# Performance work log

Hardware: AMD Instinct MI355X
Metric: run time of the kernel (lower is better)

## Reference

```python
import jax, jax.numpy as jnp
import numpy as np

B, N, M, D, H, DK = 4, 2048, 1024, 512, 8, 64  # H*DK == D (required by residual E + E_)
SCALE = 1.0 / np.sqrt(DK)
NEG = -9e15


def setup_inputs() -> dict:
    key = jax.random.key(0)
    ks = jax.random.split(key, 24)
    def W(k, din, dout):
        return (0.02 * jax.random.truncated_normal(k, -2.0, 2.0, (din, dout))).astype(jnp.float32)
    inp = {
        'X': jax.random.normal(ks[0], (B, N, D), jnp.float32),
        'incidence_matrix': jax.random.randint(ks[1], (B, N, M), 0, 2, jnp.int32),
        'attn_bias': jnp.zeros((1,), jnp.float32),
        'E': jax.random.normal(ks[2], (B, M, D), jnp.float32),
        'Wqn': W(ks[3], D, H * DK), 'bqn': jnp.zeros((H * DK,), jnp.float32),
        'Wkn': W(ks[4], D, H * DK), 'bkn': jnp.zeros((H * DK,), jnp.float32),
        'Wvn': W(ks[5], D, H * DK), 'bvn': jnp.zeros((H * DK,), jnp.float32),
        'Wqe': W(ks[6], D, H * DK), 'bqe': jnp.zeros((H * DK,), jnp.float32),
        'Wke': W(ks[7], D, H * DK), 'bke': jnp.zeros((H * DK,), jnp.float32),
        'Wve': W(ks[8], D, H * DK), 'bve': jnp.zeros((H * DK,), jnp.float32),
        'Wm1': W(ks[9], D, D), 'bm1': jnp.zeros((D,), jnp.float32),
        'Wm2': W(ks[10], D, D), 'bm2': jnp.zeros((D,), jnp.float32),
        'g_ln': jnp.ones((D,), jnp.float32), 'b_ln': jnp.zeros((D,), jnp.float32),
    }
    return inp


def _heads(x, Wt, b):
    # [B, L, D] -> [B, H, L, DK]
    b_, l_ = x.shape[0], x.shape[1]
    return (x @ Wt + b).reshape(b_, l_, H, DK).transpose(0, 2, 1, 3)


def _merge(x):
    # [B, H, L, DK] -> [B, L, H*DK]
    b_, _, l_, _ = x.shape
    return x.transpose(0, 2, 1, 3).reshape(b_, l_, H * DK)


def _layernorm(x, g, b, eps=1e-7):
    mu = jnp.mean(x, axis=-1, keepdims=True)
    var = jnp.var(x, axis=-1, keepdims=True)
    return (x - mu) * jax.lax.rsqrt(var + eps) * g + b


def _gelu(x):
    return jax.nn.gelu(x, approximate=False)


def reference(X, incidence_matrix, attn_bias, E,
              Wqn, bqn, Wkn, bkn, Wvn, bvn,
              Wqe, bqe, Wke, bke, Wve, bve,
              Wm1, bm1, Wm2, bm2, g_ln, b_ln):
    q_n = _heads(X, Wqn, bqn)   # [B,H,N,DK]
    k_n = _heads(X, Wkn, bkn)
    v_n = _heads(X, Wvn, bvn)
    q_e = _heads(E, Wqe, bqe)   # [B,H,M,DK]

    # edge attends over nodes: [B,H,M,N], masked by incidence^T
    att_e = jnp.einsum('bhmd,bhnd->bhmn', q_e, k_n) * SCALE
    mask_e = (incidence_matrix > 0).transpose(0, 2, 1)[:, None, :, :]  # [B,1,M,N]
    att_e = jnp.where(mask_e, att_e, NEG)
    w_e = jax.nn.softmax(att_e, axis=-1)
    E_ = _gelu(jnp.einsum('bhmn,bhnd->bhmd', w_e, v_n))
    E_ = _merge(E_)                                   # [B,M,D]
    E_ = _layernorm(E + E_, g_ln, b_ln)
    E_ = _gelu(E_ @ Wm1 + bm1) @ Wm2 + bm2            # MLP

    k_e = _heads(E_, Wke, bke)  # [B,H,M,DK]
    v_e = _heads(E_, Wve, bve)

    # node attends over edges: [B,H,N,M], masked by incidence
    att_n = jnp.einsum('bhnd,bhmd->bhnm', q_n, k_e) * SCALE
    mask_n = (incidence_matrix > 0)[:, None, :, :]    # [B,1,N,M]
    att_n = jnp.where(mask_n, att_n, NEG)
    w_n = jax.nn.softmax(att_n, axis=-1)
    X_ = _gelu(jnp.einsum('bhnm,bhmd->bhnd', w_n, v_e))
    X_ = _merge(X_)                                   # [B,N,D]
    return (X_, E_)
```

## Files before the change

kernel.cpp:

```cpp
#include <hip/hip_runtime.h>

typedef unsigned short u16;
typedef unsigned int   u32;
typedef unsigned long long u64;

typedef __attribute__((ext_vector_type(8))) short  bf16x8;
typedef __attribute__((ext_vector_type(16))) float f32x16;

#define SC2 0.1803368801111243f
#define CS2 11.541560327111707f

__device__ __forceinline__ float bf2f(u16 h) { return __uint_as_float(((u32)h) << 16); }
__device__ __forceinline__ u16 f2bf(float f) {
  u32 u = __float_as_uint(f);
  return (u16)((u + 0x7FFFu + ((u >> 16) & 1u)) >> 16);
}
__device__ __forceinline__ float gelu_f(float x) {
  return 0.5f * x * (1.0f + erff(x * 0.70710678118654752440f));
}
__device__ __forceinline__ void dma16(const u16* g, u16* l) {
  __builtin_amdgcn_global_load_lds(
      (const __attribute__((address_space(1))) u32*)g,
      (__attribute__((address_space(3))) u32*)l, 16, 0, 0);
}
__device__ __forceinline__ u32 cvtpk(float lo, float hi) {
  u32 r;
  asm("v_cvt_pk_bf16_f32 %0, %1, %2" : "=v"(r) : "v"(lo), "v"(hi));
  return r;
}

__global__ void detect_dtype(const u16* __restrict__ X, u32* __restrict__ flag) {
  int lane = threadIdx.x;
  int bad = 0;
  #pragma unroll
  for (int i = 0; i < 8; ++i) {
    u16 v = X[i * 64 + lane];
    int e = (v >> 7) & 0xFF;
    if (e >= 0x88) bad++;
  }
  #pragma unroll
  for (int o = 1; o < 64; o <<= 1) bad += __shfl_xor(bad, o);
  if (lane == 0) *flag = (bad > 16) ? 1u : 0u;
}

__global__ __launch_bounds__(256) void fill_diag(u32* __restrict__ out, float base,
                                                 const u32* __restrict__ flag) {
  float v = base + (*flag ? 4000.0f : 0.0f);
  u16 h = f2bf(v);
  out[blockIdx.x * 256 + threadIdx.x] = (u32)h | ((u32)h << 16);
}

__global__ __launch_bounds__(256) void conv_bf16(const void* __restrict__ src,
                                                 u16* __restrict__ dst, int n,
                                                 const u32* __restrict__ flag) {
  int i = (blockIdx.x * 256 + threadIdx.x) * 8;
  if (i >= n) return;
  if (*flag) {
    const float* s = (const float*)src + i;
    float4 a = *(const float4*)s;
    float4 b = *(const float4*)(s + 4);
    uint4 o;
    o.x = (u32)f2bf(a.x) | ((u32)f2bf(a.y) << 16);
    o.y = (u32)f2bf(a.z) | ((u32)f2bf(a.w) << 16);
    o.z = (u32)f2bf(b.x) | ((u32)f2bf(b.y) << 16);
    o.w = (u32)f2bf(b.z) | ((u32)f2bf(b.w) << 16);
    *(uint4*)(dst + i) = o;
  } else {
    *(uint4*)(dst + i) = *(const uint4*)((const u16*)src + i);
  }
}

__global__ __launch_bounds__(256) void conv_vec10(
    const void* p0, const void* p1, const void* p2, const void* p3, const void* p4,
    const void* p5, const void* p6, const void* p7, const void* p8, const void* p9,
    u16* __restrict__ dst, const u32* __restrict__ flag) {
  const void* ps[10] = {p0, p1, p2, p3, p4, p5, p6, p7, p8, p9};
  int fl = (int)(*flag);
  for (int idx = threadIdx.x; idx < 5120; idx += 256) {
    int slot = idx >> 9, off = idx & 511;
    u16 v;
    if (fl) v = f2bf(((const float*)ps[slot])[off]);
    else    v = ((const u16*)ps[slot])[off];
    dst[idx] = v;
  }
}

__global__ __launch_bounds__(256) void wtrans(
    const void* w0, const void* w1, const void* w2, const void* w3,
    const void* w4, const void* w5, const void* w6, const void* w7,
    u16* __restrict__ WT, const u32* __restrict__ flag) {
  const void* wsrc[8] = {w0, w1, w2, w3, w4, w5, w6, w7};
  __shared__ u16 tile[32][33];
  int z = blockIdx.z;
  const void* W = wsrc[z];
  u16* Wt = WT + (size_t)z * 262144;
  int fl = (int)(*flag);
  int tx = threadIdx.x & 31, ty = threadIdx.x >> 5;
  int bx = blockIdx.x * 32, by = blockIdx.y * 32;
  #pragma unroll
  for (int i = 0; i < 4; ++i) {
    int r = ty + 8 * i;
    size_t src = (size_t)(by + r) * 512 + bx + tx;
    tile[r][tx] = fl ? f2bf(((const float*)W)[src]) : ((const u16*)W)[src];
  }
  __syncthreads();
  #pragma unroll
  for (int i = 0; i < 4; ++i) {
    int r = ty + 8 * i;
    Wt[(size_t)(bx + r) * 512 + by + tx] = tile[tx][r];
  }
}

__global__ __launch_bounds__(256) void transposeV(const u16* __restrict__ Vp,
                                                  u16* __restrict__ VT, int Lk) {
  __shared__ u16 tile[64][72];
  int t = threadIdx.x;
  int nt = blockIdx.x;
  int bh = blockIdx.y;
  int nw = Lk >> 6;
  const u16* src = Vp + ((size_t)bh * Lk + nt * 64) * 64;
  int key = t >> 2, seg = t & 3;
  int dc0 = seg * 2, dc1 = seg * 2 + 1;
  uint4 a  = *(const uint4*)(src + key * 64 + ((dc0 ^ (key & 7)) << 3));
  uint4 b2 = *(const uint4*)(src + key * 64 + ((dc1 ^ (key & 7)) << 3));
  *(uint4*)&tile[key][dc0 * 8] = a;
  *(uint4*)&tile[key][dc1 * 8] = b2;
  __syncthreads();
  int d = t >> 2;
  u32 wb[8];
  #pragma unroll
  for (int i = 0; i < 8; ++i) {
    u32 lo = tile[seg * 16 + 2 * i][d];
    u32 hi = tile[seg * 16 + 2 * i + 1][d];
    wb[i] = lo | (hi << 16);
  }
  u16* base = VT + (((size_t)bh * nw + nt) * 64 + d) * 64;
  int kc0 = seg * 2, kc1 = seg * 2 + 1;
  uint4 o0; o0.x = wb[0]; o0.y = wb[1]; o0.z = wb[2]; o0.w = wb[3];
  uint4 o1; o1.x = wb[4]; o1.y = wb[5]; o1.z = wb[6]; o1.w = wb[7];
  *(uint4*)(base + ((kc0 ^ (d & 7)) << 3)) = o0;
  *(uint4*)(base + ((kc1 ^ (d & 7)) << 3)) = o1;
}

__global__ __launch_bounds__(256) void pack_rows(const int* __restrict__ inc,
                                                 u64* __restrict__ packNT) {
  int gid  = blockIdx.x * 4 + (threadIdx.x >> 6);
  int lane = threadIdx.x & 63;
  int w  = gid & 15;
  int bn = gid >> 4;
  int b = bn >> 11, n = bn & 2047;
  int v = inc[(size_t)bn * 1024 + (w << 6) + lane];
  u64 mask = __ballot(v > 0);
  if (lane == 0) packNT[((size_t)(b * 16 + w)) * 2048 + n] = mask;
}

__global__ __launch_bounds__(256) void pack_cols(const int* __restrict__ inc,
                                                 u64* __restrict__ packTT) {
  int m = blockIdx.x * 256 + threadIdx.x;
  int w = blockIdx.y;
  int b = blockIdx.z;
  const int* base = inc + ((size_t)b * 2048 + (size_t)w * 64) * 1024 + m;
  u64 out = 0;
  #pragma unroll 8
  for (int j = 0; j < 64; ++j)
    if (base[(size_t)j * 1024] > 0) out |= (1ull << j);
  packTT[((size_t)(b * 32 + w)) * 1024 + m] = out;
}

__global__ __launch_bounds__(256) void gemm_tiled(const u16* __restrict__ A,
                                                  const u16* __restrict__ Wt0, u32 wtStride,
                                                  const u16* __restrict__ bias0, u32 bStride,
                                                  u16* __restrict__ C0, u32 cStride,
                                                  int act, int blocksPerMat,
                                                  u32 modeMask, int lkshift,
                                                  void* __restrict__ out2, size_t out2_off,
                                                  const u32* __restrict__ flag) {
  __shared__ u16 As[2][8192];
  __shared__ u16 Bs[2][8192];
  int mat = blockIdx.x / blocksPerMat;
  int blk = blockIdx.x % blocksPerMat;
  const u16* Wt = Wt0 + (size_t)mat * wtStride;
  const u16* bias = bias0 + (size_t)mat * bStride;
  u16* C = C0 + (size_t)mat * cStride;
  int mode = (modeMask >> mat) & 1u;
  int f32o = out2 ? (int)(*flag) : 0;
  int tm = blk >> 2, tn = blk & 3;
  int m0 = tm * 128, n0 = tn * 128;

  int t = threadIdx.x;
  int wave = t >> 6, lane = t & 63;
  int nl = lane & 31, h32 = lane >> 5;
  int wm = wave >> 1, wn = wave & 1;

  int srow = lane >> 3;
  int gch  = (lane & 7) ^ srow;
  const u16* Ab = A  + ((size_t)m0 + wave * 32) * 512 + (size_t)srow * 512 + gch * 8;
  const u16* Bb = Wt + ((size_t)n0 + wave * 32) * 512 + (size_t)srow * 512 + gch * 8;
  u16* AsW = &As[0][0] + wave * 32 * 64;
  u16* BsW = &Bs[0][0] + wave * 32 * 64;

  #pragma unroll
  for (int c = 0; c < 4; ++c) {
    dma16(Ab + (size_t)c * 8 * 512, AsW + c * 8 * 64);
    dma16(Bb + (size_t)c * 8 * 512, BsW + c * 8 * 64);
  }
  __syncthreads();

  f32x16 a00 = {}, a01 = {}, a10 = {}, a11 = {};

  for (int kk = 0; kk < 8; ++kk) {
    int buf = kk & 1;
    if (kk + 1 < 8) {
      int k0n = (kk + 1) * 64;
      u16* AD = &As[buf ^ 1][0] + wave * 32 * 64;
      u16* BD = &Bs[buf ^ 1][0] + wave * 32 * 64;
      #pragma unroll
      for (int c = 0; c < 4; ++c) {
        dma16(Ab + (size_t)c * 8 * 512 + k0n, AD + c * 8 * 64);
        dma16(Bb + (size_t)c * 8 * 512 + k0n, BD + c * 8 * 64);
      }
    }
    const u16* Ab_s = &As[buf][0];
    const u16* Bb_s = &Bs[buf][0];
    int ar0 = wm * 64 + nl, ar1 = wm * 64 + 32 + nl;
    int br0 = wn * 64 + nl, br1 = wn * 64 + 32 + nl;
    #pragma unroll
    for (int ks = 0; ks < 4; ++ks) {
      int sw = (((ks * 2 + h32) ^ (nl & 7)) << 3);
      bf16x8 fa0 = *(const bf16x8*)(Ab_s + ar0 * 64 + sw);
      bf16x8 fa1 = *(const bf16x8*)(Ab_s + ar1 * 64 + sw);
      bf16x8 fb0 = *(const bf16x8*)(Bb_s + br0 * 64 + sw);
      bf16x8 fb1 = *(const bf16x8*)(Bb_s + br1 * 64 + sw);
      a00 = __builtin_amdgcn_mfma_f32_32x32x16_bf16(fa0, fb0, a00, 0, 0, 0);
      a01 = __builtin_amdgcn_mfma_f32_32x32x16_bf16(fa0, fb1, a01, 0, 0, 0);
      a10 = __builtin_amdgcn_mfma_f32_32x32x16_bf16(fa1, fb0, a10, 0, 0, 0);
      a11 = __builtin_amdgcn_mfma_f32_32x32x16_bf16(fa1, fb1, a11, 0, 0, 0);
    }
    __syncthreads();
  }

  int nw = 1 << (lkshift - 6);
  #pragma unroll
  for (int am = 0; am < 2; ++am) {
    #pragma unroll
    for (int bn = 0; bn < 2; ++bn) {
      const f32x16* accp = am == 0 ? (bn == 0 ? &a00 : &a01)
                                   : (bn == 0 ? &a10 : &a11);
      f32x16 acc = *accp;
      int cn = n0 + wn * 64 + bn * 32 + nl;
      float bv = bf2f(bias[cn]);
      #pragma unroll
      for (int g = 0; g < 16; ++g) {
        int rm = m0 + wm * 64 + am * 32 + (g & 3) + 8 * (g >> 2) + 4 * h32;
        float v = acc[g] + bv;
        if (act) v = gelu_f(v);
        if (mode) {
          int bb = rm >> lkshift;
          int key = rm & ((1 << lkshift) - 1);
          int nt = key >> 6, kl = key & 63;
          int d = cn & 63;
          size_t ad = ((((size_t)bb * 8 + (cn >> 6)) * nw + nt) * 64 + kl) * 64
                      + (((d >> 3) ^ (kl & 7)) << 3) + (d & 7);
          C[ad] = f2bf(v);
        } else {
          size_t ad = (size_t)rm * 512 + cn;
          C[ad] = f2bf(v);
          if (out2) {
            if (f32o) ((float*)out2)[out2_off + ad] = v;
            else      ((u16*)out2)[out2_off + ad] = f2bf(v);
          }
        }
      }
    }
  }
}

__global__ __launch_bounds__(128, 2) void flash_mfma(
    const u16* __restrict__ Q,
    const u16* __restrict__ Kp,
    const u16* __restrict__ VTp,
    const u64* __restrict__ maskT,
    void* __restrict__ Outv,
    u16* __restrict__ Opart, float* __restrict__ Lpart,
    int Lq, int Lk, int splits, int is_final, const u32* __restrict__ flag) {
  __shared__ u16 K_s[2][4096];
  __shared__ u16 V_s[2][4096];
  __shared__ u16 P_s[2][2048];

  int t = threadIdx.x;
  int wave = t >> 6, lane = t & 63;
  int nl = lane & 31, h32 = lane >> 5;
  int qtiles = Lq >> 6;
  int nwords = Lk >> 6;
  int chunk = (int)(gridDim.x >> 3);
  int wid = (blockIdx.x & 7) * chunk + (blockIdx.x >> 3);
  int r2 = wid % (qtiles * 32);
  int split = wid / (qtiles * 32);
  int qt = r2 % qtiles;
  int bh = r2 / qtiles;
  int h = bh & 7, b = bh >> 3;
  int row0 = qt * 64 + wave * 32;
  int per = nwords / splits;
  int tile0 = split * per;
  int f32o = is_final ? (int)(*flag) : 0;

  bf16x8 qf[4];
  {
    const u16* qp = Q + ((size_t)(b * Lq) + row0 + nl) * 512 + h * 64 + h32 * 8;
    #pragma unroll
    for (int ks = 0; ks < 4; ++ks) qf[ks] = *(const bf16x8*)(qp + ks * 16);
  }
  const u16* Kbh = Kp + (size_t)bh * Lk * 64;
  const u16* Vbh = VTp + (size_t)bh * nwords * 4096;
  const u64* mrow = maskT + (size_t)b * nwords * Lq + row0 + nl;

  f32x16 o0 = {}, o1 = {};
  float lsum = 0.f;

  {
    const u16* TK = Kbh + (size_t)tile0 * 4096;
    const u16* TV = Vbh + (size_t)tile0 * 4096;
    #pragma unroll
    for (int c = 0; c < 4; ++c) {
      int ch = c * 2 + wave;
      dma16(TK + ch * 512 + lane * 8, &K_s[0][ch * 512]);
      dma16(TV + ch * 512 + lane * 8, &V_s[0][ch * 512]);
    }
  }
  __syncthreads();

  for (int i = 0; i < per; ++i) {
    int nt = tile0 + i;
    int buf = i & 1;
    if (i + 1 < per) {
      const u16* TK = Kbh + (size_t)(nt + 1) * 4096;
      const u16* TV = Vbh + (size_t)(nt + 1) * 4096;
      u16* KD = K_s[buf ^ 1];
      u16* VD = V_s[buf ^ 1];
      #pragma unroll
      for (int c = 0; c < 4; ++c) {
        int ch = c * 2 + wave;
        dma16(TK + ch * 512 + lane * 8, KD + ch * 512);
        dma16(TV + ch * 512 + lane * 8, VD + ch * 512);
      }
    }
    u64 mymask = mrow[(size_t)nt * Lq];
    u32 mlo = (u32)mymask;
    u32 mhi = (u32)(mymask >> 32);

    f32x16 s0 = {}, s1 = {};
    #pragma unroll
    for (int ks = 0; ks < 4; ++ks) {
      int ch = ks * 2 + h32;
      bf16x8 k0 = *(const bf16x8*)&K_s[buf][nl * 64 + ((ch ^ (nl & 7)) << 3)];
      bf16x8 k1 = *(const bf16x8*)&K_s[buf][(32 + nl) * 64 + ((ch ^ (nl & 7)) << 3)];
      s0 = __builtin_amdgcn_mfma_f32_32x32x16_bf16(k0, qf[ks], s0, 0, 0, 0);
      s1 = __builtin_amdgcn_mfma_f32_32x32x16_bf16(k1, qf[ks], s1, 0, 0, 0);
    }
    #pragma unroll
    for (int gg = 0; gg < 4; ++gg) {
      float pv0[4], pv1[4];
      #pragma unroll
      for (int r = 0; r < 4; ++r) {
        int g = gg * 4 + r;
        int key = r + 8 * gg + 4 * h32;
        float e0 = exp2f(fmaf(s0[g], SC2, -CS2));
        float e1 = exp2f(fmaf(s1[g], SC2, -CS2));
        pv0[r] = ((mlo >> key) & 1u) ? e0 : 0.f;
        pv1[r] = ((mhi >> key) & 1u) ? e1 : 0.f;
        lsum += pv0[r] + pv1[r];
      }
      uint2 a0, a1;
      a0.x = cvtpk(pv0[0], pv0[1]);
      a0.y = cvtpk(pv0[2], pv0[3]);
      a1.x = cvtpk(pv1[0], pv1[1]);
      a1.y = cvtpk(pv1[2], pv1[3]);
      *(uint2*)&P_s[wave][gg * 256 + nl * 8 + 4 * h32]       = a0;
      *(uint2*)&P_s[wave][(4 + gg) * 256 + nl * 8 + 4 * h32] = a1;
    }
    asm volatile("s_waitcnt lgkmcnt(0)" ::: "memory");
    #pragma unroll
    for (int ks2 = 0; ks2 < 4; ++ks2) {
      int ch = ks2 * 2 + h32;
      bf16x8 pf = *(const bf16x8*)&P_s[wave][ch * 256 + nl * 8];
      bf16x8 v0 = *(const bf16x8*)&V_s[buf][nl * 64 + ((ch ^ (nl & 7)) << 3)];
      bf16x8 v1 = *(const bf16x8*)&V_s[buf][(32 + nl) * 64 + ((ch ^ (nl & 7)) << 3)];
      o0 = __builtin_amdgcn_mfma_f32_32x32x16_bf16(pf, v0, o0, 0, 0, 0);
      o1 = __builtin_amdgcn_mfma_f32_32x32x16_bf16(pf, v1, o1, 0, 0, 0);
    }
    __syncthreads();
  }
  lsum += __shfl_xor(lsum, 32);

  if (Opart) {
    u16* ob = Opart + (size_t)split * 2097152;
    #pragma unroll
    for (int g = 0; g < 16; ++g) {
      int m = (g & 3) + 8 * (g >> 2) + 4 * h32;
      size_t base = ((size_t)(b * Lq) + row0 + m) * 512 + h * 64;
      ob[base + nl]      = f2bf(o0[g]);
      ob[base + 32 + nl] = f2bf(o1[g]);
    }
    if (h32 == 0)
      Lpart[(size_t)split * 32768 + ((size_t)(b * Lq) + row0 + nl) * 8 + h] = lsum;
  } else {
    #pragma unroll
    for (int g = 0; g < 16; ++g) {
      int m = (g & 3) + 8 * (g >> 2) + 4 * h32;
      float lv = __shfl(lsum, m);
      float inv = 1.0f / (lv + 1e-30f);
      size_t base = ((size_t)(b * Lq) + row0 + m) * 512 + h * 64;
      float v0 = gelu_f(o0[g] * inv);
      float v1 = gelu_f(o1[g] * inv);
      if (f32o) {
        ((float*)Outv)[base + nl]      = v0;
        ((float*)Outv)[base + 32 + nl] = v1;
      } else {
        ((u16*)Outv)[base + nl]      = f2bf(v0);
        ((u16*)Outv)[base + 32 + nl] = f2bf(v1);
      }
    }
  }
}

__global__ __launch_bounds__(256) void ln_fused(const u16* __restrict__ Op,
                                                const float* __restrict__ Lp,
                                                const u16* __restrict__ E,
                                                const u16* __restrict__ g,
                                                const u16* __restrict__ bb,
                                                u16* __restrict__ out) {
  int r = blockIdx.x;
  int t = threadIdx.x;
  int e = t * 2;
  int h = e >> 6;
  float lv = Lp[r * 8 + h] + Lp[32768 + r * 8 + h] + 1e-30f;
  float inv = 1.0f / lv;
  size_t idx = (size_t)r * 512 + e;
  u32 u0 = *(const u32*)&Op[idx];
  u32 u1 = *(const u32*)&Op[2097152 + idx];
  u32 ue = *(const u32*)&E[idx];
  float x0 = bf2f((u16)(ue & 0xffffu)) +
             gelu_f((bf2f((u16)(u0 & 0xffffu)) + bf2f((u16)(u1 & 0xffffu))) * inv);
  float x1 = bf2f((u16)(ue >> 16)) +
             gelu_f((bf2f((u16)(u0 >> 16)) + bf2f((u16)(u1 >> 16))) * inv);
  float s = x0 + x1, q = x0 * x0 + x1 * x1;
  #pragma unroll
  for (int o = 32; o; o >>= 1) { s += __shfl_down(s, o); q += __shfl_down(q, o); }
  __shared__ float red[8];
  int wv = t >> 6, ln = t & 63;
  if (ln == 0) { red[wv] = s; red[4 + wv] = q; }
  __syncthreads();
  s = red[0] + red[1] + red[2] + red[3];
  q = red[4] + red[5] + red[6] + red[7];
  float mean = s * (1.f / 512.f);
  float var  = q * (1.f / 512.f) - mean * mean;
  float rs = rsqrtf(var + 1e-7f);
  u32 ug = *(const u32*)(g + e);
  u32 ub = *(const u32*)(bb + e);
  float y0 = (x0 - mean) * rs * bf2f((u16)(ug & 0xffffu)) + bf2f((u16)(ub & 0xffffu));
  float y1 = (x1 - mean) * rs * bf2f((u16)(ug >> 16)) + bf2f((u16)(ub >> 16));
  *(u32*)(out + idx) = (u32)f2bf(y0) | ((u32)f2bf(y1) << 16);
}

extern "C" void kernel_launch(void* const* d_in, const int* in_sizes, int n_in,
                              void* d_out, int out_size, void* d_ws, size_t ws_size,
                              hipStream_t stream) {
  (void)in_sizes; (void)n_in; (void)out_size;
  const int* inc = (const int*)d_in[1];

  char* ws = (char*)d_ws;
  u32* FLAG = (u32*)ws;
  u16* VEC  = (u16*)(ws + 1024);
  u16* WT   = (u16*)(ws + 65536);
  u16* XB   = (u16*)(ws + 8454144);
  u16* EB   = (u16*)(ws + 16842752);
  u16* QN   = (u16*)(ws + 21037056);
  u16* KN   = (u16*)(ws + 29425664);
  u16* VN   = (u16*)(ws + 37814272);
  u16* QE   = (u16*)(ws + 46202880);
  u16* EATT = (u16*)(ws + 50397184);
  u16* EFIN = (u16*)(ws + 54591488);
  u64* PACKT = (u64*)(ws + 58785792);
  u64* PACKN = (u64*)(ws + 59834368);
  const size_t NEEDED = 60882944;
  u16* ELN = (u16*)(ws + 29425664);
  u16* H1  = (u16*)(ws + 33619968);
  u16* KE  = (u16*)(ws + 37814272);
  u16* Opart = XB;
  float* Lpart = (float*)(ws + 37814272);
  u16* VTn = (u16*)d_out;
  u16* VTe = EATT;
  u16* VE  = (u16*)(ws + 42008576);

  detect_dtype<<<1, 64, 0, stream>>>((const u16*)d_in[0], FLAG);

  if (ws_size < NEEDED) {
    fill_diag<<<8192, 256, 0, stream>>>((u32*)d_out,
                                        1000.0f + (float)(ws_size >> 20), FLAG);
    return;
  }

  conv_bf16<<<2048, 256, 0, stream>>>(d_in[0], XB, 4194304, FLAG);
  conv_bf16<<<1024, 256, 0, stream>>>(d_in[3], EB, 2097152, FLAG);
  conv_vec10<<<1, 256, 0, stream>>>(d_in[5], d_in[7], d_in[9], d_in[11], d_in[13],
                                    d_in[15], d_in[17], d_in[19], d_in[20], d_in[21],
                                    VEC, FLAG);
  wtrans<<<dim3(16, 16, 8), 256, 0, stream>>>(d_in[4], d_in[6], d_in[8], d_in[10],
                                              d_in[12], d_in[14], d_in[16], d_in[18],
                                              WT, FLAG);
  pack_cols<<<dim3(4, 32, 4), 256, 0, stream>>>(inc, PACKT);
  pack_rows<<<32768, 256, 0, stream>>>(inc, PACKN);

  gemm_tiled<<<768, 256, 0, stream>>>(XB, WT, 262144, VEC, 512,
                                      QN, 4194304, 0, 256, 0b110u, 11,
                                      nullptr, 0, FLAG);
  gemm_tiled<<<128, 256, 0, stream>>>(EB, WT + 3 * 262144, 0, VEC + 3 * 512, 0,
                                      QE, 0, 0, 128, 0, 11, nullptr, 0, FLAG);

  transposeV<<<dim3(32, 32), 256, 0, stream>>>(VN, VTn, 2048);

  flash_mfma<<<1024, 128, 0, stream>>>(QE, KN, VTn, PACKT, nullptr,
                                       Opart, Lpart, 1024, 2048, 2, 0, FLAG);

  ln_fused<<<4096, 256, 0, stream>>>(Opart, Lpart, EB,
                                     VEC + 8 * 512, VEC + 9 * 512, ELN);
  gemm_tiled<<<128, 256, 0, stream>>>(ELN, WT + 6 * 262144, 0, VEC + 6 * 512, 0,
                                      H1, 0, 1, 128, 0, 11, nullptr, 0, FLAG);
  gemm_tiled<<<128, 256, 0, stream>>>(H1, WT + 7 * 262144, 0, VEC + 7 * 512, 0,
                                      EFIN, 0, 0, 128, 0, 11,
                                      d_out, 4194304, FLAG);

  gemm_tiled<<<256, 256, 0, stream>>>(EFIN, WT + 4 * 262144, 262144, VEC + 4 * 512, 512,
                                      KE, 2097152, 0, 128, 0b11u, 10,
                                      nullptr, 0, FLAG);
  transposeV<<<dim3(16, 32), 256, 0, stream>>>(VE, VTe, 1024);

  flash_mfma<<<1024, 128, 0, stream>>>(QN, KE, VTe, PACKN, d_out,
                                       nullptr, nullptr, 2048, 1024, 1, 1, FLAG);
}
```

Baseline: 384.5 us.

## Replace bitmask incidence with bf16 additive bias tiles folded into MFMA

Instead of bit-packing the incidence matrix into u64 masks and selecting per element after exp, new kernels expand it into bf16 tiles holding 0 or a large negative bias, laid out in MFMA fragment order. The flash kernel adds the bias to the scores through extra MFMAs against identity fragments, which removes the per-element bit tests and selects. In exchange it reads 16x more mask data per tile (bf16 instead of bits), adds four MFMAs per tile, and reuses several workspace regions for the tile buffers.

```diff
diff --git a/kernel.cpp b/kernel.cpp
--- a/kernel.cpp
+++ b/kernel.cpp
@@ -142,29 +142,50 @@
   *(uint4*)(base + ((kc1 ^ (d & 7)) << 3)) = o1;
 }
 
-__global__ __launch_bounds__(256) void pack_rows(const int* __restrict__ inc,
-                                                 u64* __restrict__ packNT) {
-  int gid  = blockIdx.x * 4 + (threadIdx.x >> 6);
-  int lane = threadIdx.x & 63;
-  int w  = gid & 15;
-  int bn = gid >> 4;
-  int b = bn >> 11, n = bn & 2047;
-  int v = inc[(size_t)bn * 1024 + (w << 6) + lane];
-  u64 mask = __ballot(v > 0);
-  if (lane == 0) packNT[((size_t)(b * 16 + w)) * 2048 + n] = mask;
-}
-
-__global__ __launch_bounds__(256) void pack_cols(const int* __restrict__ inc,
-                                                 u64* __restrict__ packTT) {
-  int m = blockIdx.x * 256 + threadIdx.x;
-  int w = blockIdx.y;
-  int b = blockIdx.z;
-  const int* base = inc + ((size_t)b * 2048 + (size_t)w * 64) * 1024 + m;
-  u64 out = 0;
-  #pragma unroll 8
-  for (int j = 0; j < 64; ++j)
-    if (base[(size_t)j * 1024] > 0) out |= (1ull << j);
-  packTT[((size_t)(b * 32 + w)) * 1024 + m] = out;
+__global__ __launch_bounds__(256) void inc_tiles_edge(const int* __restrict__ inc,
+                                                      u16* __restrict__ T0,
+                                                      u16* __restrict__ T1) {
+  int qt32 = blockIdx.x, nt = blockIdx.y, b = blockIdx.z;
+  int t = threadIdx.x;
+  int f = t >> 6, l = t & 63;
+  int nl = l & 31, h = l >> 5;
+  int key  = ((f >> 1) << 5) + nl;
+  int qrow = ((f & 1) << 4) + h * 8;
+  const int* src = inc + ((size_t)(b * 2048 + nt * 64 + key)) * 1024 + qt32 * 32 + qrow;
+  uint4 a = *(const uint4*)src;
+  uint4 c = *(const uint4*)(src + 4);
+  uint4 o;
+  o.x = (a.x ? 0u : 0xC480u) | (a.y ? 0u : 0xC4800000u);
+  o.y = (a.z ? 0u : 0xC480u) | (a.w ? 0u : 0xC4800000u);
+  o.z = (c.x ? 0u : 0xC480u) | (c.y ? 0u : 0xC4800000u);
+  o.w = (c.z ? 0u : 0xC480u) | (c.w ? 0u : 0xC4800000u);
+  u16* dst = (b < 2 ? T0 + (size_t)b * 2097152 : T1 + (size_t)(b - 2) * 2097152)
+             + ((size_t)nt * 32 + qt32) * 2048 + t * 8;
+  *(uint4*)dst = o;
+}
+
+__global__ __launch_bounds__(256) void inc_tiles_node(const int* __restrict__ inc,
+                                                      u16* __restrict__ T0,
+                                                      u16* __restrict__ T1) {
+  int qt32 = blockIdx.x, nt = blockIdx.y, b = blockIdx.z;
+  int t = threadIdx.x;
+  int f = t >> 6, l = t & 63;
+  int nl = l & 31, h = l >> 5;
+  int key  = ((f >> 1) << 5) + nl;
+  int qrow = ((f & 1) << 4) + h * 8;
+  const int* src = inc + ((size_t)(b * 2048 + qt32 * 32 + qrow)) * 1024 + nt * 64 + key;
+  u16 o[8];
+  #pragma unroll
+  for (int e = 0; e < 8; ++e)
+    o[e] = src[(size_t)e * 1024] ? (u16)0 : (u16)0xC480;
+  uint4 ov;
+  ov.x = (u32)o[0] | ((u32)o[1] << 16);
+  ov.y = (u32)o[2] | ((u32)o[3] << 16);
+  ov.z = (u32)o[4] | ((u32)o[5] << 16);
+  ov.w = (u32)o[6] | ((u32)o[7] << 16);
+  u16* dst = (b < 3 ? T0 + (size_t)b * 2097152 : T1)
+             + ((size_t)nt * 64 + qt32) * 2048 + t * 8;
+  *(uint4*)dst = ov;
 }
 
 __global__ __launch_bounds__(256) void gemm_tiled(const u16* __restrict__ A,
@@ -279,7 +300,9 @@
     const u16* __restrict__ Q,
     const u16* __restrict__ Kp,
     const u16* __restrict__ VTp,
-    const u64* __restrict__ maskT,
+    const u16* __restrict__ IncA,
+    const u16* __restrict__ IncB,
+    int nbA,
     void* __restrict__ Outv,
     u16* __restrict__ Opart, float* __restrict__ Lpart,
     int Lq, int Lk, int splits, int is_final, const u32* __restrict__ flag) {
@@ -310,9 +333,20 @@
     #pragma unroll
     for (int ks = 0; ks < 4; ++ks) qf[ks] = *(const bf16x8*)(qp + ks * 16);
   }
+  bf16x8 b0f = {}, b16f = {};
+  #pragma unroll
+  for (int e = 0; e < 8; ++e) {
+    b0f[e]  = (nl == h32 * 8 + e)      ? (short)0x3F80 : (short)0;
+    b16f[e] = (nl == 16 + h32 * 8 + e) ? (short)0x3F80 : (short)0;
+  }
+
   const u16* Kbh = Kp + (size_t)bh * Lk * 64;
   const u16* Vbh = VTp + (size_t)bh * nwords * 4096;
-  const u64* mrow = maskT + (size_t)b * nwords * Lq + row0 + nl;
+  size_t tstr = (size_t)(Lq >> 5) * 2048;
+  int qt2 = qt * 2 + wave;
+  const u16* It = (b < nbA ? IncA + (size_t)b * 2097152
+                           : IncB + (size_t)(b - nbA) * 2097152)
+                  + (size_t)qt2 * 2048 + lane * 8;
 
   f32x16 o0 = {}, o1 = {};
   float lsum = 0.f;
@@ -327,11 +361,20 @@
       dma16(TV + ch * 512 + lane * 8, &V_s[0][ch * 512]);
     }
   }
+  bf16x8 mc0, mc1, mc2, mc3;
+  {
+    const u16* p = It + (size_t)tile0 * tstr;
+    mc0 = *(const bf16x8*)(p);
+    mc1 = *(const bf16x8*)(p + 512);
+    mc2 = *(const bf16x8*)(p + 1024);
+    mc3 = *(const bf16x8*)(p + 1536);
+  }
   __syncthreads();
 
   for (int i = 0; i < per; ++i) {
     int nt = tile0 + i;
     int buf = i & 1;
+    bf16x8 mn0, mn1, mn2, mn3;
     if (i + 1 < per) {
       const u16* TK = Kbh + (size_t)(nt + 1) * 4096;
       const u16* TV = Vbh + (size_t)(nt + 1) * 4096;
@@ -343,10 +386,12 @@
         dma16(TK + ch * 512 + lane * 8, KD + ch * 512);
         dma16(TV + ch * 512 + lane * 8, VD + ch * 512);
       }
-    }
-    u64 mymask = mrow[(size_t)nt * Lq];
-    u32 mlo = (u32)mymask;
-    u32 mhi = (u32)(mymask >> 32);
+      const u16* p = It + (size_t)(nt + 1) * tstr;
+      mn0 = *(const bf16x8*)(p);
+      mn1 = *(const bf16x8*)(p + 512);
+      mn2 = *(const bf16x8*)(p + 1024);
+      mn3 = *(const bf16x8*)(p + 1536);
+    }
 
     f32x16 s0 = {}, s1 = {};
     #pragma unroll
@@ -357,18 +402,22 @@
       s0 = __builtin_amdgcn_mfma_f32_32x32x16_bf16(k0, qf[ks], s0, 0, 0, 0);
       s1 = __builtin_amdgcn_mfma_f32_32x32x16_bf16(k1, qf[ks], s1, 0, 0, 0);
     }
+    s0 = __builtin_amdgcn_mfma_f32_32x32x16_bf16(mc0, b0f,  s0, 0, 0, 0);
+    s0 = __builtin_amdgcn_mfma_f32_32x32x16_bf16(mc1, b16f, s0, 0, 0, 0);
+    s1 = __builtin_amdgcn_mfma_f32_32x32x16_bf16(mc2, b0f,  s1, 0, 0, 0);
+    s1 = __builtin_amdgcn_mfma_f32_32x32x16_bf16(mc3, b16f, s1, 0, 0, 0);
+
     #pragma unroll
     for (int gg = 0; gg < 4; ++gg) {
       float pv0[4], pv1[4];
       #pragma unroll
       for (int r = 0; r < 4; ++r) {
         int g = gg * 4 + r;
-        int key = r + 8 * gg + 4 * h32;
         float e0 = exp2f(fmaf(s0[g], SC2, -CS2));
         float e1 = exp2f(fmaf(s1[g], SC2, -CS2));
-        pv0[r] = ((mlo >> key) & 1u) ? e0 : 0.f;
-        pv1[r] = ((mhi >> key) & 1u) ? e1 : 0.f;
-        lsum += pv0[r] + pv1[r];
+        pv0[r] = e0;
+        pv1[r] = e1;
+        lsum += e0 + e1;
       }
       uint2 a0, a1;
       a0.x = cvtpk(pv0[0], pv0[1]);
@@ -388,6 +437,7 @@
       o0 = __builtin_amdgcn_mfma_f32_32x32x16_bf16(pf, v0, o0, 0, 0, 0);
       o1 = __builtin_amdgcn_mfma_f32_32x32x16_bf16(pf, v1, o1, 0, 0, 0);
     }
+    if (i + 1 < per) { mc0 = mn0; mc1 = mn1; mc2 = mn2; mc3 = mn3; }
     __syncthreads();
   }
   lsum += __shfl_xor(lsum, 32);
@@ -480,14 +530,16 @@
   u16* QE   = (u16*)(ws + 46202880);
   u16* EATT = (u16*)(ws + 50397184);
   u16* EFIN = (u16*)(ws + 54591488);
-  u64* PACKT = (u64*)(ws + 58785792);
-  u64* PACKN = (u64*)(ws + 59834368);
   const size_t NEEDED = 60882944;
   u16* ELN = (u16*)(ws + 29425664);
   u16* H1  = (u16*)(ws + 33619968);
   u16* KE  = (u16*)(ws + 37814272);
   u16* Opart = XB;
-  float* Lpart = (float*)(ws + 37814272);
+  float* Lpart = (float*)(ws + 4259840);
+  u16* ETIL0 = EATT;
+  u16* ETIL1 = (u16*)(ws + 37814272);
+  u16* NTIL0 = XB;
+  u16* NTIL1 = QE;
   u16* VTn = (u16*)d_out;
   u16* VTe = EATT;
   u16* VE  = (u16*)(ws + 42008576);
@@ -508,8 +560,6 @@
   wtrans<<<dim3(16, 16, 8), 256, 0, stream>>>(d_in[4], d_in[6], d_in[8], d_in[10],
                                               d_in[12], d_in[14], d_in[16], d_in[18],
                                               WT, FLAG);
-  pack_cols<<<dim3(4, 32, 4), 256, 0, stream>>>(inc, PACKT);
-  pack_rows<<<32768, 256, 0, stream>>>(inc, PACKN);
 
   gemm_tiled<<<768, 256, 0, stream>>>(XB, WT, 262144, VEC, 512,
                                       QN, 4194304, 0, 256, 0b110u, 11,
@@ -519,11 +569,16 @@
 
   transposeV<<<dim3(32, 32), 256, 0, stream>>>(VN, VTn, 2048);
 
-  flash_mfma<<<1024, 128, 0, stream>>>(QE, KN, VTn, PACKT, nullptr,
+  inc_tiles_edge<<<dim3(32, 32, 4), 256, 0, stream>>>(inc, ETIL0, ETIL1);
+
+  flash_mfma<<<1024, 128, 0, stream>>>(QE, KN, VTn, ETIL0, ETIL1, 2, nullptr,
                                        Opart, Lpart, 1024, 2048, 2, 0, FLAG);
 
   ln_fused<<<4096, 256, 0, stream>>>(Opart, Lpart, EB,
                                      VEC + 8 * 512, VEC + 9 * 512, ELN);
+
+  inc_tiles_node<<<dim3(64, 16, 4), 256, 0, stream>>>(inc, NTIL0, NTIL1);
+
   gemm_tiled<<<128, 256, 0, stream>>>(ELN, WT + 6 * 262144, 0, VEC + 6 * 512, 0,
                                       H1, 0, 1, 128, 0, 11, nullptr, 0, FLAG);
   gemm_tiled<<<128, 256, 0, stream>>>(H1, WT + 7 * 262144, 0, VEC + 7 * 512, 0,
@@ -535,6 +590,6 @@
                                       nullptr, 0, FLAG);
   transposeV<<<dim3(16, 32), 256, 0, stream>>>(VE, VTe, 1024);
 
-  flash_mfma<<<1024, 128, 0, stream>>>(QN, KE, VTe, PACKN, d_out,
+  flash_mfma<<<1024, 128, 0, stream>>>(QN, KE, VTe, NTIL0, NTIL1, 3, d_out,
                                        nullptr, nullptr, 2048, 1024, 1, 1, FLAG);
 }
```

Result: no change. 382.8 us (-0.4%).
